# Kernel optimization log

Measured on AMD Instinct MI355X. Metric: run time of the kernel, lower is better.

## Reference

```python
import jax, jax.numpy as jnp
import numpy as np

FACTOR = 2  # self.factor
KSIZE = 3   # causal_fusion depthwise conv kernel size


def causal_fusion(x, w, b):
    # x: [BH, C, N]; depthwise causal conv over the node axis (left pad k-1)
    k = w.shape[-1]
    out = jax.lax.conv_general_dilated(
        x, w, window_strides=(1,), padding=[(k - 1, 0)],
        dimension_numbers=('NCH', 'OIH', 'NCH'),
        feature_group_count=x.shape[1])
    return out + b[None, :, None]


def setup_inputs() -> dict:
    key = jax.random.key(0)
    ks = jax.random.split(key, 4)
    B, N, L, H, E = 4, 64, 128, 8, 32
    queries = jax.random.normal(ks[0], (B, N, L, H, E), jnp.float32)
    keys = jax.random.normal(ks[1], (B, N, L, H, E), jnp.float32)
    values = jax.random.normal(ks[2], (B, N, L, H, E), jnp.float32)
    attn_mask = jnp.zeros((1,), jnp.bool_)
    C = E * L  # 4096 channels seen by causal_fusion
    w_cf = jax.random.normal(ks[3], (C, 1, KSIZE), jnp.float32) * 0.05
    b_cf = jnp.zeros((C,), jnp.float32)
    return {"queries": queries, "keys": keys, "values": values,
            "attn_mask": attn_mask, "w_cf": w_cf, "b_cf": b_cf}


def reference(queries, keys, values, attn_mask, w_cf, b_cf):
    B, N, L, H, E = queries.shape  # S == L, so no pad/slice branch taken

    # --- FFT cross-correlation: corr[b,n,h,e,:] = irfft(rfft(mean_n q) * conj(rfft(k)))
    qm = jnp.broadcast_to(jnp.mean(queries, axis=1, keepdims=True), queries.shape)
    qp = jnp.transpose(qm, (0, 1, 3, 4, 2))      # [B,N,H,E,L]
    kp = jnp.transpose(keys, (0, 1, 3, 4, 2))    # [B,N,H,E,L]
    vp = jnp.transpose(values, (0, 1, 3, 4, 2))  # [B,N,H,E,L]
    corr = jnp.fft.irfft(jnp.fft.rfft(qp, axis=-1) * jnp.conj(jnp.fft.rfft(kp, axis=-1)), n=L, axis=-1)

    # --- align_speed: top-k delays over channel-mean corr, circular roll of values
    mean_corr = jnp.mean(corr, axis=3)                      # [B,N,H,L]
    weight, delay_idx = jax.lax.top_k(mean_corr, FACTOR)    # [B,N,H,F]
    delay = L - delay_idx                                   # values in [1, L]
    ar = jnp.arange(L)
    aligned = []
    for i in range(FACTOR):
        idx = (ar[None, None, None, None, :] + delay[..., i][..., None, None]) % L  # [B,N,H,1,L]
        idx = jnp.broadcast_to(idx, vp.shape)
        aligned.append(jnp.take_along_axis(vp, idx, axis=-1))  # [B,N,H,E,L]

    BH = B * H
    delay_bh = jnp.transpose(delay, (0, 2, 1, 3)).reshape(BH, N, FACTOR)
    weight_bh = jnp.transpose(weight, (0, 2, 1, 3)).reshape(BH, N, FACTOR)

    # --- per-factor: sort nodes by delay -> causal fusion over nodes -> unsort
    causal_agg = []
    for i in range(FACTOR):
        indices = jnp.argsort(delay_bh[..., i], axis=-1)               # [BH,N]
        av = jnp.transpose(aligned[i], (0, 2, 1, 3, 4)).reshape(BH, N, E, L)
        av = av * jax.nn.sigmoid(weight_bh[..., i])[:, :, None, None]
        sorted_av = jnp.take_along_axis(av, indices[:, :, None, None], axis=1)
        x = jnp.transpose(sorted_av.reshape(BH, N, E * L), (0, 2, 1))  # [BH,E*L,N]
        x = causal_fusion(x, w_cf, b_cf)
        x = jnp.transpose(x, (0, 2, 1)).reshape(BH, N, E, L)
        rev = jnp.argsort(indices, axis=-1)
        x = jnp.take_along_axis(x, rev[:, :, None, None], axis=1)
        causal_agg.append(jnp.transpose(x.reshape(B, H, N, E, L), (0, 2, 1, 3, 4)))  # [B,N,H,E,L]

    # --- align_back_speed: inverse circular shift, mean over factors
    delay_back = L - delay  # [B,N,H,F]
    agg = jnp.zeros_like(causal_agg[0])
    for i in range(FACTOR):
        idx = (ar[None, None, None, None, :] + delay_back[..., i][..., None, None]) % L
        idx = jnp.broadcast_to(idx, causal_agg[i].shape)
        agg = agg + jnp.take_along_axis(causal_agg[i], idx, axis=-1)
    agg = agg / FACTOR

    V = jnp.transpose(agg, (0, 1, 4, 2, 3))  # [B,N,L,H,E]
    return V
```

## Files before the change

kernel.cpp:

```cpp
#include <hip/hip_runtime.h>
#include <math.h>

#define B_ 4
#define N_ 64
#define L_ 128
#define H_ 8
#define E_ 32
#define SC_ 8

typedef __attribute__((ext_vector_type(8))) short short8;
typedef __attribute__((ext_vector_type(4))) float f32x4;

__device__ __forceinline__ unsigned short f2bf(float x) {
    union { float f; unsigned u; } c; c.f = x;
    unsigned r = (c.u + 0x7fffu + ((c.u >> 16) & 1u)) >> 16;
    return (unsigned short)r;
}
__device__ __forceinline__ float bf2f(unsigned short h) {
    union { unsigned u; float f; } c; c.u = ((unsigned)h) << 16;
    return c.f;
}

__global__ __launch_bounds__(256) void k_qmean(const float* __restrict__ q,
                                               float* __restrict__ qm) {
    int blk = blockIdx.x;
    int b = blk >> 7, t = blk & 127;
    int c = threadIdx.x;
    const float* p = q + (((size_t)(b * N_)) * L_ + t) * 256 + c;
    double s = 0.0;
    for (int n = 0; n < N_; ++n) s += (double)p[(size_t)n * L_ * 256];
    qm[((size_t)b * 256 + c) * L_ + t] = (float)(s * (1.0 / 64.0));
}

__global__ void k_prepwb(const float* __restrict__ w, const float* __restrict__ bias,
                         float* __restrict__ wT, float* __restrict__ bT) {
    int k = blockIdx.x * 256 + threadIdx.x;
    int e = k & 31, lp = k >> 5;
    int c = e * L_ + lp;
    wT[k]          = w[c * 3 + 0];
    wT[4096 + k]   = w[c * 3 + 1];
    wT[8192 + k]   = w[c * 3 + 2];
    bT[k]          = bias[c];
}

__global__ __launch_bounds__(512) void k_corr(const float* __restrict__ keys,
                                              const float* __restrict__ qm,
                                              float* __restrict__ part) {
    int blk = blockIdx.x;
    int sc = blk & 7; int bh = blk >> 3; int h = bh & 7; int b = bh >> 3;
    __shared__ unsigned short Ahi[4][64][40];
    __shared__ unsigned short Alo[4][64][40];
    __shared__ unsigned short Qhi[128][40];
    __shared__ unsigned short Qlo[128][40];
    int tid = threadIdx.x;
    int lane = tid & 63, w = tid >> 6;
    int mg = w & 1, ng = w >> 1;

    {
        int e = tid >> 4; int tq = (tid & 15) * 4;
        const float* qp = qm + ((size_t)b * 256 + h * 32 + e) * 128;
        #pragma unroll
        for (int hf = 0; hf < 2; ++hf) {
            int t0 = tq + hf * 64;
            float4 v = *(const float4*)(qp + t0);
            float vv[4] = {v.x, v.y, v.z, v.w};
            #pragma unroll
            for (int j = 0; j < 4; ++j) {
                unsigned short hi = f2bf(vv[j]);
                Qhi[t0 + j][e] = hi;
                Qlo[t0 + j][e] = f2bf(vv[j] - bf2f(hi));
            }
        }
    }
    int sn = tid >> 3; int se = (tid & 7) * 4;
    const float* kbase = keys + ((size_t)(b * N_ + sn) * L_) * 256 + h * 32 + se;
    #pragma unroll
    for (int p = 0; p < 2; ++p) {
        float4 v = *(const float4*)(kbase + (size_t)(sc * 16 + p) * 256);
        float vv[4] = {v.x, v.y, v.z, v.w};
        ushort4 h4, l4;
        unsigned short* hp = (unsigned short*)&h4;
        unsigned short* lp = (unsigned short*)&l4;
        #pragma unroll
        for (int j = 0; j < 4; ++j) {
            hp[j] = f2bf(vv[j]);
            lp[j] = f2bf(vv[j] - bf2f(hp[j]));
        }
        *(ushort4*)&Ahi[p][sn][se] = h4;
        *(ushort4*)&Alo[p][sn][se] = l4;
    }
    __syncthreads();

    f32x4 acc[2][2];
    #pragma unroll
    for (int i = 0; i < 2; ++i)
        #pragma unroll
        for (int j = 0; j < 2; ++j)
            acc[i][j] = (f32x4){0.f, 0.f, 0.f, 0.f};

    int eb = (lane >> 4) * 8;
    int rA0 = (mg * 2) * 16 + (lane & 15);
    int rA1 = rA0 + 16;
    int tau0 = (ng * 2) * 16 + (lane & 15);
    int tau1 = tau0 + 16;

    for (int it = 0; it < 8; ++it) {
        float4 stg0, stg1;
        if (it < 7) {
            stg0 = *(const float4*)(kbase + (size_t)(sc * 16 + 2 * it + 2) * 256);
            stg1 = *(const float4*)(kbase + (size_t)(sc * 16 + 2 * it + 3) * 256);
        }
        #pragma unroll
        for (int sp = 0; sp < 2; ++sp) {
            int p = 2 * it + sp;
            int slot = p & 3;
            int s = sc * 16 + p;
            short8 ah0 = *(const short8*)&Ahi[slot][rA0][eb];
            short8 ah1 = *(const short8*)&Ahi[slot][rA1][eb];
            short8 al0 = *(const short8*)&Alo[slot][rA0][eb];
            short8 al1 = *(const short8*)&Alo[slot][rA1][eb];
            int t0 = (s + tau0) & 127;
            int t1 = (s + tau1) & 127;
            short8 bh0 = *(const short8*)&Qhi[t0][eb];
            short8 bh1 = *(const short8*)&Qhi[t1][eb];
            short8 bl0 = *(const short8*)&Qlo[t0][eb];
            short8 bl1 = *(const short8*)&Qlo[t1][eb];
            acc[0][0] = __builtin_amdgcn_mfma_f32_16x16x32_bf16(ah0, bh0, acc[0][0], 0, 0, 0);
            acc[0][1] = __builtin_amdgcn_mfma_f32_16x16x32_bf16(ah0, bh1, acc[0][1], 0, 0, 0);
            acc[1][0] = __builtin_amdgcn_mfma_f32_16x16x32_bf16(ah1, bh0, acc[1][0], 0, 0, 0);
            acc[1][1] = __builtin_amdgcn_mfma_f32_16x16x32_bf16(ah1, bh1, acc[1][1], 0, 0, 0);
            acc[0][0] = __builtin_amdgcn_mfma_f32_16x16x32_bf16(ah0, bl0, acc[0][0], 0, 0, 0);
            acc[0][1] = __builtin_amdgcn_mfma_f32_16x16x32_bf16(ah0, bl1, acc[0][1], 0, 0, 0);
            acc[1][0] = __builtin_amdgcn_mfma_f32_16x16x32_bf16(ah1, bl0, acc[1][0], 0, 0, 0);
            acc[1][1] = __builtin_amdgcn_mfma_f32_16x16x32_bf16(ah1, bl1, acc[1][1], 0, 0, 0);
            acc[0][0] = __builtin_amdgcn_mfma_f32_16x16x32_bf16(al0, bh0, acc[0][0], 0, 0, 0);
            acc[0][1] = __builtin_amdgcn_mfma_f32_16x16x32_bf16(al0, bh1, acc[0][1], 0, 0, 0);
            acc[1][0] = __builtin_amdgcn_mfma_f32_16x16x32_bf16(al1, bh0, acc[1][0], 0, 0, 0);
            acc[1][1] = __builtin_amdgcn_mfma_f32_16x16x32_bf16(al1, bh1, acc[1][1], 0, 0, 0);
        }
        if (it < 7) {
            #pragma unroll
            for (int sp = 0; sp < 2; ++sp) {
                int p = 2 * it + 2 + sp;
                int slot = p & 3;
                float4 v = sp ? stg1 : stg0;
                float vv[4] = {v.x, v.y, v.z, v.w};
                ushort4 h4, l4;
                unsigned short* hp = (unsigned short*)&h4;
                unsigned short* lp = (unsigned short*)&l4;
                #pragma unroll
                for (int j = 0; j < 4; ++j) {
                    hp[j] = f2bf(vv[j]);
                    lp[j] = f2bf(vv[j] - bf2f(hp[j]));
                }
                *(ushort4*)&Ahi[slot][sn][se] = h4;
                *(ushort4*)&Alo[slot][sn][se] = l4;
            }
        }
        __syncthreads();
    }

    #pragma unroll
    for (int i = 0; i < 2; ++i) {
        int mt = mg * 2 + i;
        #pragma unroll
        for (int j = 0; j < 2; ++j) {
            int nt = ng * 2 + j;
            int tau = nt * 16 + (lane & 15);
            #pragma unroll
            for (int r = 0; r < 4; ++r) {
                int n = mt * 16 + (lane >> 4) * 4 + r;
                part[((((size_t)sc * B_ + b) * N_ + n) * H_ + h) * L_ + tau] = acc[i][j][r];
            }
        }
    }
}

__global__ __launch_bounds__(64) void k_topk(const float* __restrict__ part,
                                             int* __restrict__ didx,
                                             float* __restrict__ sig,
                                             int* __restrict__ flags) {
    int blk = blockIdx.x;
    int lane = threadIdx.x;
    size_t rb = (size_t)blk * L_;
    const size_t stride = (size_t)B_ * N_ * H_ * L_;
    double s0 = 0.0, s1 = 0.0;
    for (int sc = 0; sc < SC_; ++sc) {
        s0 += (double)part[sc * stride + rb + lane];
        s1 += (double)part[sc * stride + rb + lane + 64];
    }
    float v0 = (float)(s0 * (1.0 / 32.0));
    float v1 = (float)(s1 * (1.0 / 32.0));

    float bv = v0; int bi = lane;
    if (v1 > v0) { bv = v1; bi = lane + 64; }
    #pragma unroll
    for (int m = 32; m; m >>= 1) {
        float ov = __shfl_xor(bv, m, 64);
        int   oi = __shfl_xor(bi, m, 64);
        if (ov > bv || (ov == bv && oi < bi)) { bv = ov; bi = oi; }
    }
    int i1 = bi; float w1v = bv;

    float c0 = (lane == i1) ? -INFINITY : v0;
    float c1 = (lane + 64 == i1) ? -INFINITY : v1;
    float bv2 = c0; int bi2 = lane;
    if (c1 > c0) { bv2 = c1; bi2 = lane + 64; }
    #pragma unroll
    for (int m = 32; m; m >>= 1) {
        float ov = __shfl_xor(bv2, m, 64);
        int   oi = __shfl_xor(bi2, m, 64);
        if (ov > bv2 || (ov == bv2 && oi < bi2)) { bv2 = ov; bi2 = oi; }
    }
    int i2 = bi2; float w2v = bv2;

    float d0 = (lane == i1 || lane == i2) ? -INFINITY : v0;
    float d1 = (lane + 64 == i1 || lane + 64 == i2) ? -INFINITY : v1;
    float bv3 = fmaxf(d0, d1);
    #pragma unroll
    for (int m = 32; m; m >>= 1) bv3 = fmaxf(bv3, __shfl_xor(bv3, m, 64));

    if (lane == 0) {
        didx[blk * 2 + 0] = i1;
        didx[blk * 2 + 1] = i2;
        sig[blk * 2 + 0] = 1.f / (1.f + expf(-w1v));
        sig[blk * 2 + 1] = 1.f / (1.f + expf(-w2v));
        flags[blk] = (w2v - bv3 < 1e-3f) ? 1 : 0;
    }
}

__global__ __launch_bounds__(256) void k_fixup(const float* __restrict__ keys,
                                               const float* __restrict__ qm,
                                               const int* __restrict__ flags,
                                               double* __restrict__ vvg) {
    int row = blockIdx.x >> 3; int tg = blockIdx.x & 7;
    if (!flags[row]) return;
    int h = row & 7; int r = row >> 3; int n = r & 63; int b = r >> 6;
    __shared__ float ks_t[L_][E_];
    __shared__ float qs_t[L_][E_];
    __shared__ double red[16][17];
    int tid = threadIdx.x;
    for (int idx = tid; idx < 1024; idx += 256) {
        int s = idx >> 3, e4 = idx & 7;
        *(float4*)&ks_t[s][e4 * 4] =
            *(const float4*)&keys[(((size_t)(b * N_ + n)) * L_ + s) * 256 + h * E_ + e4 * 4];
        int e = idx >> 5, t4 = (idx & 31) * 4;
        float4 v = *(const float4*)&qm[((size_t)b * 256 + h * E_ + e) * L_ + t4];
        float vvj[4] = {v.x, v.y, v.z, v.w};
        #pragma unroll
        for (int j = 0; j < 4; ++j) {
            int t = t4 + j;
            int col = ((((e >> 2) ^ (t & 7)) << 2) | (e & 3));
            qs_t[t][col] = vvj[j];
        }
    }
    __syncthreads();
    int tau = tg * 16 + (tid & 15);
    int g = tid >> 4;
    double a0 = 0, a1 = 0, a2 = 0, a3 = 0, a4 = 0, a5 = 0, a6 = 0, a7 = 0;
    #pragma unroll 2
    for (int s = g * 8; s < g * 8 + 8; ++s) {
        int t = (s + tau) & 127;
        int x = t & 7;
        #pragma unroll
        for (int e4 = 0; e4 < 8; e4 += 2) {
            float4 k0 = *(const float4*)&ks_t[s][e4 * 4];
            float4 k1 = *(const float4*)&ks_t[s][e4 * 4 + 4];
            float4 q0 = *(const float4*)&qs_t[t][(e4 ^ x) << 2];
            float4 q1 = *(const float4*)&qs_t[t][((e4 + 1) ^ x) << 2];
            a0 = fma((double)k0.x, (double)q0.x, a0);
            a1 = fma((double)k0.y, (double)q0.y, a1);
            a2 = fma((double)k0.z, (double)q0.z, a2);
            a3 = fma((double)k0.w, (double)q0.w, a3);
            a4 = fma((double)k1.x, (double)q1.x, a4);
            a5 = fma((double)k1.y, (double)q1.y, a5);
            a6 = fma((double)k1.z, (double)q1.z, a6);
            a7 = fma((double)k1.w, (double)q1.w, a7);
        }
    }
    red[g][tid & 15] = ((a0 + a1) + (a2 + a3)) + ((a4 + a5) + (a6 + a7));
    __syncthreads();
    if (tid < 16) {
        double s = 0;
        #pragma unroll
        for (int gg = 0; gg < 16; ++gg) s += red[gg][tid];
        vvg[(size_t)row * L_ + tg * 16 + tid] = s;
    }
}

__global__ __launch_bounds__(128) void k_sort(int* __restrict__ didx,
                                              float* __restrict__ sig,
                                              const int* __restrict__ flags,
                                              const double* __restrict__ vvg,
                                              int* __restrict__ pred) {
    int bh = blockIdx.x;
    int b = bh >> 3, h = bh & 7;
    int tid = threadIdx.x; int i = tid >> 6; int n = tid & 63;
    __shared__ int ds[2][64];
    __shared__ int pm[2][64];
    ds[i][n] = 128 - didx[((b * 64 + n) * 8 + h) * 2 + i];
    __syncthreads();

    if (tid < 64) {
        int lane = tid;
        for (int nn = 0; nn < 64; ++nn) {
            int row = ((b * 64 + nn) * 8 + h);
            if (!flags[row]) continue;
            float v0 = (float)(vvg[(size_t)row * L_ + lane] * (1.0 / 32.0));
            float v1 = (float)(vvg[(size_t)row * L_ + lane + 64] * (1.0 / 32.0));
            float bv = v0; int bi = lane;
            if (v1 > v0) { bv = v1; bi = lane + 64; }
            #pragma unroll
            for (int m = 32; m; m >>= 1) {
                float ov = __shfl_xor(bv, m, 64);
                int   oi = __shfl_xor(bi, m, 64);
                if (ov > bv || (ov == bv && oi < bi)) { bv = ov; bi = oi; }
            }
            int i1 = bi; float w1v = bv;
            float c0 = (lane == i1) ? -INFINITY : v0;
            float c1 = (lane + 64 == i1) ? -INFINITY : v1;
            float bv2 = c0; int bi2 = lane;
            if (c1 > c0) { bv2 = c1; bi2 = lane + 64; }
            #pragma unroll
            for (int m = 32; m; m >>= 1) {
                float ov = __shfl_xor(bv2, m, 64);
                int   oi = __shfl_xor(bi2, m, 64);
                if (ov > bv2 || (ov == bv2 && oi < bi2)) { bv2 = ov; bi2 = oi; }
            }
            if (lane == 0) {
                didx[row * 2 + 0] = i1;
                didx[row * 2 + 1] = bi2;
                sig[row * 2 + 0] = 1.f / (1.f + expf(-w1v));
                sig[row * 2 + 1] = 1.f / (1.f + expf(-bv2));
                ds[0][nn] = 128 - i1;
                ds[1][nn] = 128 - bi2;
            }
        }
    }
    __syncthreads();

    int d = ds[i][n];
    int rank = 0;
    for (int m = 0; m < 64; ++m) {
        int dm = ds[i][m];
        rank += (dm < d || (dm == d && m < n)) ? 1 : 0;
    }
    pm[i][rank] = n;
    __syncthreads();
    int p1v = (rank >= 1) ? pm[i][rank - 1] : -1;
    int p2v = (rank >= 2) ? pm[i][rank - 2] : -1;
    int o = ((bh * 2 + i) * 64 + n) * 2;
    pred[o] = p1v; pred[o + 1] = p2v;
}

__global__ __launch_bounds__(256, 2) void k_out(const float* __restrict__ values,
                                                const float* __restrict__ wT,
                                                const float* __restrict__ bT,
                                                const int* __restrict__ didx,
                                                const float* __restrict__ sig,
                                                const int* __restrict__ pred,
                                                float* __restrict__ out) {
    int bid = blockIdx.x;
    int half = bid & 1; int blk = bid >> 1;
    int h = blk & 7; int r = blk >> 3; int n = r & 63; int b = r >> 6;
    int tid = threadIdx.x; int e4 = tid & 7; int tq = tid >> 3;

    int di[2]; float si[2];
    int pq1[2], pq2[2], dq1[2], dq2[2]; float s1[2], s2[2];
    #pragma unroll
    for (int i = 0; i < 2; ++i) {
        di[i] = didx[blk * 2 + i];
        si[i] = sig[blk * 2 + i];
        int po = (((b * 8 + h) * 2 + i) * 64 + n) * 2;
        int p1 = pred[po], p2 = pred[po + 1];
        if (p1 >= 0) { int q = ((b * 64 + p1) * 8 + h) * 2 + i; pq1[i] = p1; dq1[i] = didx[q]; s1[i] = sig[q]; }
        else         { pq1[i] = n; dq1[i] = di[i]; s1[i] = 0.f; }
        if (p2 >= 0) { int q = ((b * 64 + p2) * 8 + h) * 2 + i; pq2[i] = p2; dq2[i] = didx[q]; s2[i] = sig[q]; }
        else         { pq2[i] = n; dq2[i] = di[i]; s2[i] = 0.f; }
    }
    const f32x4* v4 = (const f32x4*)values;
    const f32x4* w4 = (const f32x4*)wT;
    const f32x4* b4 = (const f32x4*)bT;
    f32x4* o4 = (f32x4*)out;
    const size_t base = ((size_t)b * N_) * L_ * 64 + h * 8 + e4;

    f32x4 vs[2], va1[2], va2[2], vb1[2], vb2[2];
    int lp0[2], lp1[2];
    #pragma unroll
    for (int it = 0; it < 2; ++it) {
        int t = half * 64 + tq + 32 * it;
        vs[it] = v4[base + ((size_t)n * L_ + t) * 64];
        int ta1 = (t + di[0] - dq1[0]) & 127;
        va1[it] = v4[base + ((size_t)pq1[0] * L_ + ta1) * 64];
        int ta2 = (t + di[0] - dq2[0]) & 127;
        va2[it] = v4[base + ((size_t)pq2[0] * L_ + ta2) * 64];
        int tb1 = (t + di[1] - dq1[1]) & 127;
        vb1[it] = v4[base + ((size_t)pq1[1] * L_ + tb1) * 64];
        int tb2 = (t + di[1] - dq2[1]) & 127;
        vb2[it] = v4[base + ((size_t)pq2[1] * L_ + tb2) * 64];
        lp0[it] = (t + di[0]) & 127;
        lp1[it] = (t + di[1]) & 127;
    }
    f32x4 bb0[2], w0a[2], w1a[2], w2a[2], bb1[2], w0b[2], w1b[2], w2b[2];
    #pragma unroll
    for (int it = 0; it < 2; ++it) {
        int wo0 = lp0[it] * 8 + e4, wo1 = lp1[it] * 8 + e4;
        bb0[it] = b4[wo0]; w0a[it] = w4[wo0]; w1a[it] = w4[1024 + wo0]; w2a[it] = w4[2048 + wo0];
        bb1[it] = b4[wo1]; w0b[it] = w4[wo1]; w1b[it] = w4[1024 + wo1]; w2b[it] = w4[2048 + wo1];
    }
    #pragma unroll
    for (int it = 0; it < 2; ++it) {
        int t = half * 64 + tq + 32 * it;
        f32x4 acc = bb0[it] + bb1[it];
        acc += w2a[it] * (si[0] * vs[it]);
        acc += w1a[it] * (s1[0] * va1[it]);
        acc += w0a[it] * (s2[0] * va2[it]);
        acc += w2b[it] * (si[1] * vs[it]);
        acc += w1b[it] * (s1[1] * vb1[it]);
        acc += w0b[it] * (s2[1] * vb2[it]);
        o4[base + ((size_t)n * L_ + t) * 64] = acc * 0.5f;
    }
}

extern "C" void kernel_launch(void* const* d_in, const int* in_sizes, int n_in,
                              void* d_out, int out_size, void* d_ws, size_t ws_size,
                              hipStream_t stream) {
    const float* queries = (const float*)d_in[0];
    const float* keys    = (const float*)d_in[1];
    const float* values  = (const float*)d_in[2];
    const float* w_cf = (const float*)d_in[4];
    const float* b_cf = (const float*)d_in[5];
    float* out = (float*)d_out;

    float* ws    = (float*)d_ws;
    float* qm    = ws;
    float* wT    = qm + 131072;
    float* bT    = wT + 12288;
    float* sigp  = bT + 4096;
    int*   didxp = (int*)(sigp + 4096);
    int*   predp = didxp + 4096;
    int*   flags = predp + 8192;
    double* vvg  = (double*)(flags + 2048);

    float* part = (float*)d_out;

    k_qmean <<<512,  256, 0, stream>>>(queries, qm);
    k_prepwb<<<16,   256, 0, stream>>>(w_cf, b_cf, wT, bT);
    k_corr  <<<256,  512, 0, stream>>>(keys, qm, part);
    k_topk  <<<2048, 64,  0, stream>>>(part, didxp, sigp, flags);
    k_fixup <<<16384, 256, 0, stream>>>(keys, qm, flags, vvg);
    k_sort  <<<32,   128, 0, stream>>>(didxp, sigp, flags, vvg, predp);
    k_out   <<<4096, 256, 0, stream>>>(values, wT, bT, didxp, sigp, predp, out);
}
```

Before: 82.12 us.

## Fuse weight prep into qmean, vectorize qmean, ballot-skip sort rows, remap k_out blocks

```diff
diff --git a/kernel.cpp b/kernel.cpp
--- a/kernel.cpp
+++ b/kernel.cpp
@@ -22,25 +22,42 @@
 }
 
 __global__ __launch_bounds__(256) void k_qmean(const float* __restrict__ q,
-                                               float* __restrict__ qm) {
+                                               float* __restrict__ qm,
+                                               const float* __restrict__ w,
+                                               const float* __restrict__ bias,
+                                               float* __restrict__ wT,
+                                               float* __restrict__ bT) {
     int blk = blockIdx.x;
     int b = blk >> 7, t = blk & 127;
-    int c = threadIdx.x;
-    const float* p = q + (((size_t)(b * N_)) * L_ + t) * 256 + c;
-    double s = 0.0;
-    for (int n = 0; n < N_; ++n) s += (double)p[(size_t)n * L_ * 256];
+    int tid = threadIdx.x;
+    int c4 = tid & 63;
+    int nq = tid >> 6;
+    __shared__ double red[4][256];
+    const f32x4* p = (const f32x4*)(q + (((size_t)(b * N_)) * L_ + t) * 256);
+    double s0 = 0, s1 = 0, s2 = 0, s3 = 0;
+    #pragma unroll 4
+    for (int n = nq * 16; n < nq * 16 + 16; ++n) {
+        f32x4 v = p[(size_t)n * 8192 + c4];
+        s0 += (double)v.x; s1 += (double)v.y; s2 += (double)v.z; s3 += (double)v.w;
+    }
+    red[nq][c4 * 4 + 0] = s0;
+    red[nq][c4 * 4 + 1] = s1;
+    red[nq][c4 * 4 + 2] = s2;
+    red[nq][c4 * 4 + 3] = s3;
+    __syncthreads();
+    int c = tid;
+    double s = red[0][c] + red[1][c] + red[2][c] + red[3][c];
     qm[((size_t)b * 256 + c) * L_ + t] = (float)(s * (1.0 / 64.0));
-}
-
-__global__ void k_prepwb(const float* __restrict__ w, const float* __restrict__ bias,
-                         float* __restrict__ wT, float* __restrict__ bT) {
-    int k = blockIdx.x * 256 + threadIdx.x;
-    int e = k & 31, lp = k >> 5;
-    int c = e * L_ + lp;
-    wT[k]          = w[c * 3 + 0];
-    wT[4096 + k]   = w[c * 3 + 1];
-    wT[8192 + k]   = w[c * 3 + 2];
-    bT[k]          = bias[c];
+
+    if (blk < 16) {
+        int k = blk * 256 + tid;
+        int e = k & 31, lp = k >> 5;
+        int cc = e * L_ + lp;
+        wT[k]        = w[cc * 3 + 0];
+        wT[4096 + k] = w[cc * 3 + 1];
+        wT[8192 + k] = w[cc * 3 + 2];
+        bT[k]        = bias[cc];
+    }
 }
 
 __global__ __launch_bounds__(512) void k_corr(const float* __restrict__ keys,
@@ -303,9 +320,11 @@
 
     if (tid < 64) {
         int lane = tid;
-        for (int nn = 0; nn < 64; ++nn) {
-            int row = ((b * 64 + nn) * 8 + h);
-            if (!flags[row]) continue;
+        int myflag = flags[(b * 64 + lane) * 8 + h];
+        unsigned long long msk = __ballot(myflag != 0);
+        while (msk) {
+            int nn = __ffsll((long long)msk) - 1; msk &= msk - 1;
+            int row = (b * 64 + nn) * 8 + h;
             float v0 = (float)(vvg[(size_t)row * L_ + lane] * (1.0 / 32.0));
             float v1 = (float)(vvg[(size_t)row * L_ + lane + 64] * (1.0 / 32.0));
             float bv = v0; int bi = lane;
@@ -361,8 +380,11 @@
                                                 const int* __restrict__ pred,
                                                 float* __restrict__ out) {
     int bid = blockIdx.x;
-    int half = bid & 1; int blk = bid >> 1;
-    int h = blk & 7; int r = blk >> 3; int n = r & 63; int b = r >> 6;
+    int h = bid & 7;
+    int b = bid >> 10;
+    int j = (bid >> 3) & 127;
+    int n = j >> 1; int half = j & 1;
+    int blk = (b * 64 + n) * 8 + h;
     int tid = threadIdx.x; int e4 = tid & 7; int tq = tid >> 3;
 
     int di[2]; float si[2];
@@ -444,11 +466,10 @@
 
     float* part = (float*)d_out;
 
-    k_qmean <<<512,  256, 0, stream>>>(queries, qm);
-    k_prepwb<<<16,   256, 0, stream>>>(w_cf, b_cf, wT, bT);
-    k_corr  <<<256,  512, 0, stream>>>(keys, qm, part);
-    k_topk  <<<2048, 64,  0, stream>>>(part, didxp, sigp, flags);
+    k_qmean <<<512,   256, 0, stream>>>(queries, qm, w_cf, b_cf, wT, bT);
+    k_corr  <<<256,   512, 0, stream>>>(keys, qm, part);
+    k_topk  <<<2048,  64,  0, stream>>>(part, didxp, sigp, flags);
     k_fixup <<<16384, 256, 0, stream>>>(keys, qm, flags, vvg);
-    k_sort  <<<32,   128, 0, stream>>>(didxp, sigp, flags, vvg, predp);
-    k_out   <<<4096, 256, 0, stream>>>(values, wT, bT, didxp, sigp, predp, out);
-}
+    k_sort  <<<32,    128, 0, stream>>>(didxp, sigp, flags, vvg, predp);
+    k_out   <<<4096,  256, 0, stream>>>(values, wT, bT, didxp, sigp, predp, out);
+}
```

After: 77.27 us. -5.9%, faster.
